# Optimization experiments

Measured on AMD Instinct MI355X. Metric: run time of the kernel, lower is better.

The kernel has to match this reference:

```python
import jax, jax.numpy as jnp
import numpy as np

B, C, H, W = 4, 64, 64, 64
C2 = 2 * C
CR = C2 // 16  # SE bottleneck

def setup_inputs() -> dict:
    key = jax.random.key(0)
    ks = jax.random.split(key, 8)
    stdv = 1.0 / np.sqrt(C)
    return {
        "x1": jax.random.normal(ks[0], (B, C, H, W), jnp.float32),
        "x2": jax.random.normal(ks[1], (B, C, H, W), jnp.float32),
        "weight": jax.random.uniform(ks[2], (C, C), jnp.float32, -stdv, stdv),
        "weight2": jax.random.uniform(ks[3], (C, C), jnp.float32, -stdv, stdv),
        "ca_fc1": jax.random.normal(ks[4], (CR, C2), jnp.float32) * 0.05,  # 1x1 conv as matrix
        "ca_fc2": jax.random.normal(ks[5], (C2, CR), jnp.float32) * 0.05,
        "conv_w": jax.random.normal(ks[6], (C, C2), jnp.float32) * 0.05,  # 1x1 conv 2C->C
        "conv_b": jnp.zeros((C,), jnp.float32),
    }

def reference(x1, x2, weight, weight2, ca_fc1, ca_fc2, conv_w, conv_b):
    b, c, h, w = x2.shape
    n = h * w
    a1 = x1.reshape(b, c, n)  # x1 flattened [B,C,N]
    a2 = x2.reshape(b, c, n)  # x2 flattened [B,C,N]
    # Non-local branch: f = theta_x @ phi_x = a1^T @ a2 -> [B,N,N]
    f = jnp.einsum('bcn,bcm->bnm', a1, a2)
    adj = jax.nn.softmax(f, axis=-1)
    support = jnp.einsum('bcn,cd->bnd', a2, weight)  # g_x @ W, [B,N,C]
    y = jnp.einsum('bnm,bmd->bnd', adj, support)     # adj @ support
    y = y.transpose(0, 2, 1).reshape(b, c, h, w)
    # Channel-affinity branch: c_x = a_x @ b_x -> [B,C,C]
    c_x = jnp.einsum('bcn,bdn->bcd', a1, a2)
    support2 = jnp.einsum('bcd,de->bce', c_x, weight2)   # [B,C,C]
    y2 = jnp.einsum('bcd,bdn->bcn', support2, a1).reshape(b, c, h, w)
    z = jnp.concatenate([y, y2], axis=1)  # [B,2C,H,W]
    # ChannelAttention: global max pool -> fc1 -> relu -> fc2 -> sigmoid
    mp = jnp.max(z, axis=(2, 3))                       # [B,2C]
    hdn = jax.nn.relu(jnp.einsum('be,re->br', mp, ca_fc1))
    v = jax.nn.sigmoid(jnp.einsum('br,er->be', hdn, ca_fc2))  # [B,2C]
    out = z * v[:, :, None, None] + z
    out = jnp.einsum('behw,oe->bohw', out, conv_w) + conv_b[None, :, None, None]
    return out
```

## Files before the change

kernel.cpp:

```cpp
#include <hip/hip_runtime.h>
#include <hip/hip_bf16.h>
#include <math.h>

#define B_   4
#define C_   64
#define N_   4096
#define C2_  128

using frag  = __attribute__((ext_vector_type(8))) short;
using f32x4 = __attribute__((ext_vector_type(4))) float;
using f4    = __attribute__((ext_vector_type(4))) float;

__device__ __forceinline__ unsigned short f2bf(float f) {
  unsigned int u = __float_as_uint(f);
  u += 0x7fffu + ((u >> 16) & 1u);
  return (unsigned short)(u >> 16);
}
__device__ __forceinline__ float bf2f(unsigned short h) {
  return __uint_as_float(((unsigned int)h) << 16);
}
__device__ __forceinline__ unsigned int pkbf(float a, float b) {
  __hip_bfloat16 ha = __float2bfloat16(a), hb = __float2bfloat16(b);
  unsigned short ua, ub;
  __builtin_memcpy(&ua, &ha, 2);
  __builtin_memcpy(&ub, &hb, 2);
  return (unsigned int)ua | ((unsigned int)ub << 16);
}
__device__ __forceinline__ frag pk8(f4 lo, f4 hi) {
  frag f;
  unsigned int* u = (unsigned int*)&f;
  u[0] = pkbf(lo.x, lo.y);
  u[1] = pkbf(lo.z, lo.w);
  u[2] = pkbf(hi.x, hi.y);
  u[3] = pkbf(hi.z, hi.w);
  return f;
}
__device__ __forceinline__ f4 max4(f4 a, f4 b) {
  return (f4){fmaxf(a.x, b.x), fmaxf(a.y, b.y), fmaxf(a.z, b.z), fmaxf(a.w, b.w)};
}

__global__ __launch_bounds__(256) void prep_kernel(const float* __restrict__ x1,
                                                   const float* __restrict__ x2,
                                                   const float* __restrict__ weight,
                                                   unsigned short* __restrict__ a1t,
                                                   unsigned short* __restrict__ a2t,
                                                   unsigned short* __restrict__ vT) {
  __shared__ float tileA[64][65];
  __shared__ float tileB[64][65];
  __shared__ float Wl[64 * 64];
  int b = blockIdx.y, n0 = blockIdx.x * 64, tid = threadIdx.x;
  int n = tid & 63;
#pragma unroll
  for (int k = 0; k < 16; ++k) {
    int lin = tid + 256 * k;
    Wl[lin] = weight[lin];
    int c = (tid >> 6) + 4 * k;
    tileA[c][n] = x2[((size_t)(b * C_ + c)) * N_ + n0 + n];
    tileB[c][n] = x1[((size_t)(b * C_ + c)) * N_ + n0 + n];
  }
  __syncthreads();
  {
    int c = tid & 63;
#pragma unroll
    for (int k = 0; k < 16; ++k) {
      int n2 = (tid >> 6) + 4 * k;
      a2t[((size_t)b * N_ + n0 + n2) * C_ + c] = f2bf(tileA[c][n2]);
      a1t[((size_t)b * N_ + n0 + n2) * C_ + c] = f2bf(tileB[c][n2]);
    }
  }
  {
    int d0 = (tid >> 6) * 16;
    float acc[16];
#pragma unroll
    for (int i = 0; i < 16; ++i) acc[i] = 0.f;
    for (int c = 0; c < 64; ++c) {
      float v = tileA[c][n];
#pragma unroll
      for (int i = 0; i < 16; ++i) acc[i] += v * Wl[c * 64 + d0 + i];
    }
#pragma unroll
    for (int i = 0; i < 16; ++i)
      vT[((size_t)(b * C_) + d0 + i) * N_ + n0 + n] = f2bf(acc[i]);
  }
}

__global__ __launch_bounds__(256) void cxmm_kernel(const float* __restrict__ x1,
                                                   const float* __restrict__ x2,
                                                   float* __restrict__ cxp) {
  int b = blockIdx.y, seg = blockIdx.x, tid = threadIdx.x;
  int wave = tid >> 6, lane = tid & 63, l16 = lane & 15, lq = lane >> 4;
  int n0 = seg * 64;
  const float* a2r = x2 + ((size_t)(b * C_) + 16 * wave + l16) * N_ + n0 + lq * 8;
  frag afr[2];
#pragma unroll
  for (int ks = 0; ks < 2; ++ks)
    afr[ks] = pk8(*(const f4*)(a2r + ks * 32), *(const f4*)(a2r + ks * 32 + 4));
  f32x4 acc[4];
#pragma unroll
  for (int cg = 0; cg < 4; ++cg) acc[cg] = (f32x4){0.f, 0.f, 0.f, 0.f};
#pragma unroll
  for (int cg = 0; cg < 4; ++cg) {
    const float* a1r = x1 + ((size_t)(b * C_) + cg * 16 + l16) * N_ + n0 + lq * 8;
#pragma unroll
    for (int ks = 0; ks < 2; ++ks) {
      frag bfr = pk8(*(const f4*)(a1r + ks * 32), *(const f4*)(a1r + ks * 32 + 4));
      acc[cg] = __builtin_amdgcn_mfma_f32_16x16x32_bf16(afr[ks], bfr, acc[cg], 0, 0, 0);
    }
  }
  float* op = cxp + ((size_t)(b * 64 + seg)) * 4096;
#pragma unroll
  for (int cg = 0; cg < 4; ++cg)
#pragma unroll
    for (int r = 0; r < 4; ++r)
      op[(16 * wave + 4 * lq + r) * 64 + cg * 16 + l16] = acc[cg][r];
}

__global__ __launch_bounds__(256) void cxred_kernel(const float* __restrict__ cxp,
                                                    float* __restrict__ cx) {
  int idx = blockIdx.x * 256 + threadIdx.x;
  int b = idx >> 12, r = idx & 4095;
  const float* p = cxp + (size_t)b * 64 * 4096 + r;
  float s = 0.f;
#pragma unroll 8
  for (int sg = 0; sg < 64; ++sg) s += p[(size_t)sg * 4096];
  cx[idx] = s;
}

__global__ __launch_bounds__(256) void s2bf_kernel(const float* __restrict__ cx,
                                                   const float* __restrict__ w2,
                                                   unsigned short* __restrict__ s2bf) {
  __shared__ float cxl[4096];
  __shared__ float w2l[4096];
  int b = blockIdx.x, tid = threadIdx.x;
#pragma unroll
  for (int k = 0; k < 16; ++k) {
    int lin = tid + 256 * k;
    cxl[lin] = cx[(size_t)b * 4096 + lin];
    w2l[lin] = w2[lin];
  }
  __syncthreads();
  int c = tid & 63, eg = tid >> 6;
  float acc[16];
#pragma unroll
  for (int i = 0; i < 16; ++i) acc[i] = 0.f;
  for (int d = 0; d < 64; ++d) {
    float a = cxl[d * 64 + c];
#pragma unroll
    for (int i = 0; i < 16; ++i) acc[i] += a * w2l[d * 64 + eg * 16 + i];
  }
  unsigned short* op = s2bf + (size_t)b * 4096 + c * 64 + eg * 16;
#pragma unroll
  for (int i = 0; i < 8; ++i)
    *(unsigned int*)(op + 2 * i) = pkbf(acc[2 * i], acc[2 * i + 1]);
}

template <int SEG>
__global__ __launch_bounds__(256) void attn_kernel(const unsigned short* __restrict__ a1t,
                                                   const unsigned short* __restrict__ a2t,
                                                   const unsigned short* __restrict__ vT,
                                                   float* __restrict__ z,
                                                   unsigned short* __restrict__ Opart,
                                                   float* __restrict__ ml) {
  __shared__ unsigned short Kt[2][64 * 64];
  __shared__ unsigned short Vt[2][64 * 64];
  __shared__ uint2 Pl[4][16 * 16];

  const int b = blockIdx.y, n0 = blockIdx.x * 64, tid = threadIdx.x;
  const int seg = (SEG > 1) ? blockIdx.z : 0;
  const int wave = tid >> 6, lane = tid & 63;
  const int l16 = lane & 15, lq = lane >> 4;
  const int NT = N_ / SEG / 64;
  const int mbase = seg * (N_ / SEG);

  const unsigned short* qbase = a1t + ((size_t)b * N_ + n0 + wave * 16 + l16) * C_;
  frag qa0 = *(const frag*)(qbase + lq * 8);
  frag qa1 = *(const frag*)(qbase + 32 + lq * 8);

  f32x4 O[4];
#pragma unroll
  for (int i = 0; i < 4; ++i) O[i] = (f32x4){0.f, 0.f, 0.f, 0.f};
  float m_l = -1e30f, l_l = 0.f;

  const unsigned short* a2b = a2t + (size_t)b * N_ * C_;
  const unsigned short* vTb = vT + (size_t)b * C_ * N_;
  char* Pw = (char*)&Pl[wave][0];
  const int swzP = (l16 & 7) << 4;

  const int srow0 = tid >> 3, scb = tid & 7;
  const int srow1 = (tid + 256) >> 3;
  const int kswz0 = (scb * 16) ^ ((srow0 & 7) << 4);
  const int kswz1 = (scb * 16) ^ ((srow1 & 7) << 4);

  frag k0 = *(const frag*)(a2b + (size_t)(mbase + srow0) * C_ + scb * 8);
  frag k1 = *(const frag*)(a2b + (size_t)(mbase + srow1) * C_ + scb * 8);
  frag v0 = *(const frag*)(vTb + (size_t)srow0 * N_ + mbase + scb * 8);
  frag v1 = *(const frag*)(vTb + (size_t)srow1 * N_ + mbase + scb * 8);
  *(frag*)((char*)&Kt[0][0] + srow0 * 128 + kswz0) = k0;
  *(frag*)((char*)&Kt[0][0] + srow1 * 128 + kswz1) = k1;
  *(frag*)((char*)&Vt[0][0] + srow0 * 128 + kswz0) = v0;
  *(frag*)((char*)&Vt[0][0] + srow1 * 128 + kswz1) = v1;
  __syncthreads();

  int cur = 0;
  for (int t = 0; t < NT; ++t, cur ^= 1) {
    if (t + 1 < NT) {
      int mn = mbase + (t + 1) * 64;
      k0 = *(const frag*)(a2b + (size_t)(mn + srow0) * C_ + scb * 8);
      k1 = *(const frag*)(a2b + (size_t)(mn + srow1) * C_ + scb * 8);
      v0 = *(const frag*)(vTb + (size_t)srow0 * N_ + mn + scb * 8);
      v1 = *(const frag*)(vTb + (size_t)srow1 * N_ + mn + scb * 8);
    }

    f32x4 S[4];
    __builtin_amdgcn_s_setprio(1);
#pragma unroll
    for (int ms = 0; ms < 4; ++ms) {
      int m = ms * 16 + l16;
      int swz = (m & 7) << 4;
      frag kb0 = *(const frag*)((char*)&Kt[cur][0] + m * 128 + ((lq * 16) ^ swz));
      frag kb1 = *(const frag*)((char*)&Kt[cur][0] + m * 128 + ((64 + lq * 16) ^ swz));
      f32x4 acc = (f32x4){0.f, 0.f, 0.f, 0.f};
      acc = __builtin_amdgcn_mfma_f32_16x16x32_bf16(kb0, qa0, acc, 0, 0, 0);
      acc = __builtin_amdgcn_mfma_f32_16x16x32_bf16(kb1, qa1, acc, 0, 0, 0);
      S[ms] = acc;
    }
    __builtin_amdgcn_s_setprio(0);

    float mx0 = fmaxf(fmaxf(S[0][0], S[0][1]), fmaxf(S[0][2], S[0][3]));
    float mx1 = fmaxf(fmaxf(S[1][0], S[1][1]), fmaxf(S[1][2], S[1][3]));
    float mx2 = fmaxf(fmaxf(S[2][0], S[2][1]), fmaxf(S[2][2], S[2][3]));
    float mx3 = fmaxf(fmaxf(S[3][0], S[3][1]), fmaxf(S[3][2], S[3][3]));
    float mx = fmaxf(fmaxf(mx0, mx1), fmaxf(mx2, mx3));
    mx = fmaxf(mx, __shfl_xor(mx, 16, 64));
    mx = fmaxf(mx, __shfl_xor(mx, 32, 64));

    if (!__all(mx <= m_l + 8.f)) {
      float mn = fmaxf(m_l, mx);
      float sc = __expf(m_l - mn);
      m_l = mn;
      l_l *= sc;
      float scb_[4];
#pragma unroll
      for (int r = 0; r < 4; ++r) scb_[r] = __shfl(sc, 20 * lq + r, 64);
#pragma unroll
      for (int ds = 0; ds < 4; ++ds)
#pragma unroll
        for (int r = 0; r < 4; ++r) O[ds][r] *= scb_[r];
    }

    float p[16];
    float rs = 0.f;
#pragma unroll
    for (int ms = 0; ms < 4; ++ms)
#pragma unroll
      for (int r = 0; r < 4; ++r) {
        float e = __expf(S[ms][r] - m_l);
        p[ms * 4 + r] = e;
        rs += e;
      }
    rs += __shfl_xor(rs, 16, 64);
    rs += __shfl_xor(rs, 32, 64);
    l_l += rs;

#pragma unroll
    for (int ms = 0; ms < 4; ++ms) {
      uint2 w;
      w.x = pkbf(p[ms * 4 + 0], p[ms * 4 + 1]);
      w.y = pkbf(p[ms * 4 + 2], p[ms * 4 + 3]);
      *(uint2*)(Pw + l16 * 128 + ((32 * ms + 8 * lq) ^ swzP)) = w;
    }
    asm volatile("s_waitcnt lgkmcnt(0)" ::: "memory");
    __builtin_amdgcn_sched_barrier(0);

    frag pa0 = *(const frag*)(Pw + l16 * 128 + ((lq * 16) ^ swzP));
    frag pa1 = *(const frag*)(Pw + l16 * 128 + ((64 + lq * 16) ^ swzP));
    __builtin_amdgcn_s_setprio(1);
#pragma unroll
    for (int ds = 0; ds < 4; ++ds) {
      int d = ds * 16 + l16;
      int swz = (d & 7) << 4;
      frag vb0 = *(const frag*)((char*)&Vt[cur][0] + d * 128 + ((lq * 16) ^ swz));
      frag vb1 = *(const frag*)((char*)&Vt[cur][0] + d * 128 + ((64 + lq * 16) ^ swz));
      O[ds] = __builtin_amdgcn_mfma_f32_16x16x32_bf16(pa0, vb0, O[ds], 0, 0, 0);
      O[ds] = __builtin_amdgcn_mfma_f32_16x16x32_bf16(pa1, vb1, O[ds], 0, 0, 0);
    }
    __builtin_amdgcn_s_setprio(0);

    if (t + 1 < NT) {
      *(frag*)((char*)&Kt[cur ^ 1][0] + srow0 * 128 + kswz0) = k0;
      *(frag*)((char*)&Kt[cur ^ 1][0] + srow1 * 128 + kswz1) = k1;
      *(frag*)((char*)&Vt[cur ^ 1][0] + srow0 * 128 + kswz0) = v0;
      *(frag*)((char*)&Vt[cur ^ 1][0] + srow1 * 128 + kswz1) = v1;
      __syncthreads();
    }
  }

  if (SEG > 1) {
    size_t base = (size_t)(b * SEG + seg) * N_ + n0 + wave * 16;
    if (lq == 0) {
      ml[(base + l16) * 2]     = m_l;
      ml[(base + l16) * 2 + 1] = l_l;
    }
#pragma unroll
    for (int r = 0; r < 4; ++r)
#pragma unroll
      for (int ds = 0; ds < 4; ++ds)
        Opart[(base + lq * 4 + r) * 64 + ds * 16 + l16] = f2bf(O[ds][r]);
  } else {
    float inv[4];
#pragma unroll
    for (int r = 0; r < 4; ++r) inv[r] = 1.f / __shfl(l_l, 20 * lq + r, 64);
#pragma unroll
    for (int ds = 0; ds < 4; ++ds)
#pragma unroll
      for (int r = 0; r < 4; ++r)
        z[((size_t)b * N_ + n0 + wave * 16 + lq * 4 + r) * 128 + ds * 16 + l16] = O[ds][r] * inv[r];
  }
}

__global__ __launch_bounds__(256) void combine_kernel(const unsigned short* __restrict__ Opart,
                                                      const float* __restrict__ ml,
                                                      float* __restrict__ z,
                                                      float* __restrict__ mppA) {
  __shared__ float zsm[64][65];
  int b = blockIdx.y, tid = threadIdx.x;
  int nr = tid >> 2;
  int n = blockIdx.x * 64 + nr;
  int dq = (tid & 3) * 16;
  float mv[4], lv[4], M = -1e30f;
#pragma unroll
  for (int s = 0; s < 4; ++s) {
    size_t r = (size_t)(b * 4 + s) * N_ + n;
    mv[s] = ml[r * 2];
    lv[s] = ml[r * 2 + 1];
    M = fmaxf(M, mv[s]);
  }
  float acc[16];
#pragma unroll
  for (int j = 0; j < 16; ++j) acc[j] = 0.f;
  float l = 0.f;
#pragma unroll
  for (int s = 0; s < 4; ++s) {
    float w = __expf(mv[s] - M);
    l += w * lv[s];
    const unsigned short* op = Opart + ((size_t)(b * 4 + s) * N_ + n) * 64 + dq;
    frag p0 = *(const frag*)(op);
    frag p1 = *(const frag*)(op + 8);
#pragma unroll
    for (int j = 0; j < 8; ++j) {
      acc[j]     += w * bf2f((unsigned short)p0[j]);
      acc[8 + j] += w * bf2f((unsigned short)p1[j]);
    }
  }
  float inv = 1.f / l;
  float* zp = z + ((size_t)b * N_ + n) * 128 + dq;
#pragma unroll
  for (int k = 0; k < 4; ++k) {
    f4 res = (f4){acc[4 * k] * inv, acc[4 * k + 1] * inv,
                  acc[4 * k + 2] * inv, acc[4 * k + 3] * inv};
    *(f4*)(zp + k * 4) = res;
    zsm[nr][dq + 4 * k]     = res.x;
    zsm[nr][dq + 4 * k + 1] = res.y;
    zsm[nr][dq + 4 * k + 2] = res.z;
    zsm[nr][dq + 4 * k + 3] = res.w;
  }
  __syncthreads();
  if (tid < 64) {
    float mx = -1e30f;
    for (int nn = 0; nn < 64; ++nn) mx = fmaxf(mx, zsm[nn][tid]);
    mppA[((size_t)b * 64 + blockIdx.x) * 64 + tid] = mx;
  }
}

__global__ __launch_bounds__(256) void mpA_kernel(const float* __restrict__ z,
                                                  float* __restrict__ mppA) {
  __shared__ float red[4][64];
  int b = blockIdx.y, n0 = blockIdx.x * 64, tid = threadIdx.x;
  int e = tid & 63, g = tid >> 6;
  float mx = -1e30f;
#pragma unroll
  for (int k = 0; k < 16; ++k)
    mx = fmaxf(mx, z[((size_t)b * N_ + n0 + g + 4 * k) * 128 + e]);
  red[g][e] = mx;
  __syncthreads();
  if (tid < 64)
    mppA[((size_t)b * 64 + blockIdx.x) * 64 + tid] =
        fmaxf(fmaxf(red[0][tid], red[1][tid]), fmaxf(red[2][tid], red[3][tid]));
}

__global__ __launch_bounds__(256) void y2_kernel(const unsigned short* __restrict__ s2bf,
                                                 const unsigned short* __restrict__ a1t,
                                                 float* __restrict__ z,
                                                 float* __restrict__ mppB) {
  __shared__ f4 red[4][4][16];
  int b = blockIdx.y, n0 = blockIdx.x * 32, tid = threadIdx.x;
  int wave = tid >> 6, lane = tid & 63, l16 = lane & 15, lq = lane >> 4;
  const unsigned short* s2r = s2bf + (size_t)b * 4096 + (16 * wave + l16) * 64;
  frag sa0 = *(const frag*)(s2r + lq * 8);
  frag sa1 = *(const frag*)(s2r + 32 + lq * 8);
  f4 mx = (f4){-1e30f, -1e30f, -1e30f, -1e30f};
#pragma unroll
  for (int j = 0; j < 2; ++j) {
    const unsigned short* bp = a1t + ((size_t)b * N_ + n0 + 16 * j + l16) * 64;
    frag b0 = *(const frag*)(bp + lq * 8);
    frag b1 = *(const frag*)(bp + 32 + lq * 8);
    f32x4 acc = (f32x4){0.f, 0.f, 0.f, 0.f};
    acc = __builtin_amdgcn_mfma_f32_16x16x32_bf16(sa0, b0, acc, 0, 0, 0);
    acc = __builtin_amdgcn_mfma_f32_16x16x32_bf16(sa1, b1, acc, 0, 0, 0);
    *(f4*)(z + ((size_t)b * N_ + n0 + 16 * j + l16) * 128 + 64 + 16 * wave + 4 * lq) = acc;
#pragma unroll
    for (int r = 0; r < 4; ++r) mx[r] = fmaxf(mx[r], acc[r]);
  }
  red[wave][lq][l16] = mx;
  __syncthreads();
  if (tid < 64) {
    int w = tid >> 4, q = (tid >> 2) & 3, r = tid & 3;
    float m = -1e30f;
#pragma unroll
    for (int l = 0; l < 16; ++l) m = fmaxf(m, red[w][q][l][r]);
    mppB[((size_t)b * 128 + blockIdx.x) * 64 + 16 * w + 4 * q + r] = m;
  }
}

__global__ __launch_bounds__(256) void ca2_kernel(const float* __restrict__ mppA,
                                                  const float* __restrict__ mppB,
                                                  const float* __restrict__ fc1,
                                                  const float* __restrict__ fc2,
                                                  float* __restrict__ vbuf) {
  __shared__ f4 red4[256];
  __shared__ float mpl[128];
  __shared__ float red2[8][33];
  __shared__ float hl[8];
  int b = blockIdx.x, t = threadIdx.x;
  {
    const f4* src = (const f4*)(mppA + (size_t)b * 64 * 64);
    f4 m = src[t];
    m = max4(m, src[t + 256]);
    m = max4(m, src[t + 512]);
    m = max4(m, src[t + 768]);
    red4[t] = m;
  }
  __syncthreads();
  if (t < 16) {
    f4 m = red4[t];
#pragma unroll
    for (int j = 1; j < 16; ++j) m = max4(m, red4[t + 16 * j]);
    *(f4*)&mpl[t * 4] = m;
  }
  __syncthreads();
  {
    const f4* src = (const f4*)(mppB + (size_t)b * 128 * 64);
    f4 m = src[t];
#pragma unroll
    for (int k = 1; k < 8; ++k) m = max4(m, src[t + 256 * k]);
    red4[t] = m;
  }
  __syncthreads();
  if (t < 16) {
    f4 m = red4[t];
#pragma unroll
    for (int j = 1; j < 16; ++j) m = max4(m, red4[t + 16 * j]);
    *(f4*)&mpl[64 + t * 4] = m;
  }
  __syncthreads();
  {
    int r = t >> 5, j = t & 31;
    const f4 mv = *(const f4*)&mpl[j * 4];
    const f4 wv = *(const f4*)(fc1 + r * 128 + j * 4);
    red2[r][j] = mv.x * wv.x + mv.y * wv.y + mv.z * wv.z + mv.w * wv.w;
  }
  __syncthreads();
  if (t < 8) {
    float s = 0.f;
#pragma unroll
    for (int j = 0; j < 32; ++j) s += red2[t][j];
    hl[t] = fmaxf(s, 0.f);
  }
  __syncthreads();
  if (t < 128) {
    float s = 0.f;
    const float* f2r = fc2 + t * 8;
#pragma unroll
    for (int r = 0; r < 8; ++r) s += hl[r] * f2r[r];
    vbuf[b * 128 + t] = 1.f + 1.f / (1.f + __expf(-s));
  }
}

__global__ __launch_bounds__(256) void conv_kernel(const float* __restrict__ z,
                                                   const float* __restrict__ vbuf,
                                                   const float* __restrict__ conv_w,
                                                   const float* __restrict__ conv_b,
                                                   float* __restrict__ out) {
  __shared__ unsigned short zv[64 * 128];
  int b = blockIdx.y, n0 = blockIdx.x * 64, tid = threadIdx.x;
  int wave = tid >> 6, lane = tid & 63, l16 = lane & 15, lq = lane >> 4;
  {
    int e4 = tid & 31;
    f4 vq = *(const f4*)(vbuf + b * 128 + e4 * 4);
#pragma unroll
    for (int k = 0; k < 8; ++k) {
      int row = (tid >> 5) + 8 * k;
      f4 zq = *(const f4*)(z + ((size_t)(b * N_) + n0 + row) * 128 + e4 * 4);
      zq *= vq;
      uint2 w;
      w.x = pkbf(zq.x, zq.y);
      w.y = pkbf(zq.z, zq.w);
      *(uint2*)((char*)zv + row * 256 + ((e4 * 8) ^ ((row & 7) << 4))) = w;
    }
  }
  const float* cwr = conv_w + (size_t)(16 * wave + l16) * 128 + lq * 8;
  frag aw[4];
#pragma unroll
  for (int ks = 0; ks < 4; ++ks)
    aw[ks] = pk8(*(const f4*)(cwr + ks * 32), *(const f4*)(cwr + ks * 32 + 4));
  __syncthreads();
  f32x4 acc[4];
#pragma unroll
  for (int ng = 0; ng < 4; ++ng) acc[ng] = (f32x4){0.f, 0.f, 0.f, 0.f};
#pragma unroll
  for (int ng = 0; ng < 4; ++ng) {
    int n = ng * 16 + l16;
    int swz = (n & 7) << 4;
#pragma unroll
    for (int ks = 0; ks < 4; ++ks) {
      frag bz = *(const frag*)((char*)zv + n * 256 + ((ks * 64 + lq * 16) ^ swz));
      acc[ng] = __builtin_amdgcn_mfma_f32_16x16x32_bf16(aw[ks], bz, acc[ng], 0, 0, 0);
    }
  }
#pragma unroll
  for (int r = 0; r < 4; ++r) {
    int o = 16 * wave + 4 * lq + r;
    float bias = conv_b[o];
#pragma unroll
    for (int ng = 0; ng < 4; ++ng)
      out[((size_t)(b * C_ + o)) * N_ + n0 + ng * 16 + l16] = acc[ng][r] + bias;
  }
}

extern "C" void kernel_launch(void* const* d_in, const int* in_sizes, int n_in,
                              void* d_out, int out_size, void* d_ws, size_t ws_size,
                              hipStream_t stream) {
  const float* x1      = (const float*)d_in[0];
  const float* x2      = (const float*)d_in[1];
  const float* weight  = (const float*)d_in[2];
  const float* weight2 = (const float*)d_in[3];
  const float* fc1     = (const float*)d_in[4];
  const float* fc2     = (const float*)d_in[5];
  const float* conv_w  = (const float*)d_in[6];
  const float* conv_b  = (const float*)d_in[7];
  float* out = (float*)d_out;

  char* ws = (char*)d_ws;
  unsigned short* a1t = (unsigned short*)(ws + 0);
  unsigned short* a2t = (unsigned short*)(ws + 2097152);
  float* mppA = (float*)(ws + 2097152);
  float* mppB = (float*)(ws + 2162688);
  unsigned short* s2bf = (unsigned short*)(ws + 2293760);
  unsigned short* vT  = (unsigned short*)(ws + 4194304);
  float* z    = (float*)(ws + 6291456);
  float* cxp  = (float*)(ws + 6291456);
  float* cx   = (float*)(ws + 14680064);
  float* vbuf = (float*)(ws + 14745600);
  unsigned short* Opart = (unsigned short*)(ws + 14764544);
  float* ml   = (float*)(ws + 23153152);
  const bool seg4 = ws_size >= 23677440ull;

  cxmm_kernel<<<dim3(64, 4), 256, 0, stream>>>(x1, x2, cxp);
  prep_kernel<<<dim3(64, 4), 256, 0, stream>>>(x1, x2, weight, a1t, a2t, vT);
  cxred_kernel<<<dim3(64), 256, 0, stream>>>(cxp, cx);
  if (seg4) {
    attn_kernel<4><<<dim3(64, 4, 4), 256, 0, stream>>>(a1t, a2t, vT, z, Opart, ml);
    combine_kernel<<<dim3(64, 4), 256, 0, stream>>>(Opart, ml, z, mppA);
  } else {
    attn_kernel<1><<<dim3(64, 4), 256, 0, stream>>>(a1t, a2t, vT, z, nullptr, nullptr);
    mpA_kernel<<<dim3(64, 4), 256, 0, stream>>>(z, mppA);
  }
  s2bf_kernel<<<dim3(4), 256, 0, stream>>>(cx, weight2, s2bf);
  y2_kernel<<<dim3(128, 4), 256, 0, stream>>>(s2bf, a1t, z, mppB);
  ca2_kernel<<<dim3(4), 256, 0, stream>>>(mppA, mppB, fc1, fc2, vbuf);
  conv_kernel<<<dim3(64, 4), 256, 0, stream>>>(z, vbuf, conv_w, conv_b, out);
}
```

Before: 83.29 us.

## Split prep into transpose kernel and MFMA-based support matmul kernel

The fused prep kernel previously transposed x1/x2 to bf16 and computed x2^T·W with scalar FMAs from shared memory. It is now split into a lighter transpose kernel with half-size tiles (more blocks) and a separate kernel that computes the support product with bf16 MFMA instructions reading the transposed a2t. This aims to remove the scalar FMA loop and raise parallelism, at the cost of an extra launch, a re-read of a2t, and bf16 rounding of W and x2 before the product.

```diff
diff --git a/kernel.cpp b/kernel.cpp
--- a/kernel.cpp
+++ b/kernel.cpp
@@ -41,47 +41,73 @@
 
 __global__ __launch_bounds__(256) void prep_kernel(const float* __restrict__ x1,
                                                    const float* __restrict__ x2,
-                                                   const float* __restrict__ weight,
                                                    unsigned short* __restrict__ a1t,
-                                                   unsigned short* __restrict__ a2t,
-                                                   unsigned short* __restrict__ vT) {
-  __shared__ float tileA[64][65];
-  __shared__ float tileB[64][65];
-  __shared__ float Wl[64 * 64];
-  int b = blockIdx.y, n0 = blockIdx.x * 64, tid = threadIdx.x;
-  int n = tid & 63;
+                                                   unsigned short* __restrict__ a2t) {
+  __shared__ float tA[64 * 33];
+  __shared__ float tB[64 * 33];
+  int b = blockIdx.y, n0 = blockIdx.x * 32, tid = threadIdx.x;
+  {
+    int n = tid & 31, cq = tid >> 5;
+#pragma unroll
+    for (int k = 0; k < 8; ++k) {
+      int c = cq + 8 * k;
+      tA[c * 33 + n] = x2[((size_t)(b * C_ + c)) * N_ + n0 + n];
+      tB[c * 33 + n] = x1[((size_t)(b * C_ + c)) * N_ + n0 + n];
+    }
+  }
+  __syncthreads();
+  {
+    int c = tid & 63, nq = tid >> 6;
+#pragma unroll
+    for (int k = 0; k < 8; ++k) {
+      int n2 = nq + 4 * k;
+      a2t[((size_t)b * N_ + n0 + n2) * C_ + c] = f2bf(tA[c * 33 + n2]);
+      a1t[((size_t)b * N_ + n0 + n2) * C_ + c] = f2bf(tB[c * 33 + n2]);
+    }
+  }
+}
+
+__global__ __launch_bounds__(256) void support_mm_kernel(const float* __restrict__ weight,
+                                                         const unsigned short* __restrict__ a2t,
+                                                         unsigned short* __restrict__ vT) {
+  __shared__ float Wl[64 * 65];
+  int b = blockIdx.y, n0 = blockIdx.x * 32, tid = threadIdx.x;
+  int wave = tid >> 6, lane = tid & 63, l16 = lane & 15, lq = lane >> 4;
 #pragma unroll
   for (int k = 0; k < 16; ++k) {
     int lin = tid + 256 * k;
-    Wl[lin] = weight[lin];
-    int c = (tid >> 6) + 4 * k;
-    tileA[c][n] = x2[((size_t)(b * C_ + c)) * N_ + n0 + n];
-    tileB[c][n] = x1[((size_t)(b * C_ + c)) * N_ + n0 + n];
-  }
-  __syncthreads();
-  {
-    int c = tid & 63;
-#pragma unroll
-    for (int k = 0; k < 16; ++k) {
-      int n2 = (tid >> 6) + 4 * k;
-      a2t[((size_t)b * N_ + n0 + n2) * C_ + c] = f2bf(tileA[c][n2]);
-      a1t[((size_t)b * N_ + n0 + n2) * C_ + c] = f2bf(tileB[c][n2]);
-    }
-  }
-  {
-    int d0 = (tid >> 6) * 16;
-    float acc[16];
-#pragma unroll
-    for (int i = 0; i < 16; ++i) acc[i] = 0.f;
-    for (int c = 0; c < 64; ++c) {
-      float v = tileA[c][n];
-#pragma unroll
-      for (int i = 0; i < 16; ++i) acc[i] += v * Wl[c * 64 + d0 + i];
-    }
-#pragma unroll
-    for (int i = 0; i < 16; ++i)
-      vT[((size_t)(b * C_) + d0 + i) * N_ + n0 + n] = f2bf(acc[i]);
-  }
+    Wl[(lin >> 6) * 65 + (lin & 63)] = weight[lin];
+  }
+  frag b0[2], b1[2];
+#pragma unroll
+  for (int ng = 0; ng < 2; ++ng) {
+    const unsigned short* bp = a2t + ((size_t)b * N_ + n0 + ng * 16 + l16) * C_;
+    b0[ng] = *(const frag*)(bp + lq * 8);
+    b1[ng] = *(const frag*)(bp + 32 + lq * 8);
+  }
+  __syncthreads();
+  int dd = 16 * wave + l16;
+  frag aw[2];
+#pragma unroll
+  for (int ks = 0; ks < 2; ++ks) {
+    float wv[8];
+#pragma unroll
+    for (int j = 0; j < 8; ++j) wv[j] = Wl[(ks * 32 + lq * 8 + j) * 65 + dd];
+    aw[ks] = pk8((f4){wv[0], wv[1], wv[2], wv[3]}, (f4){wv[4], wv[5], wv[6], wv[7]});
+  }
+  f32x4 acc[2];
+#pragma unroll
+  for (int ng = 0; ng < 2; ++ng) {
+    acc[ng] = (f32x4){0.f, 0.f, 0.f, 0.f};
+    acc[ng] = __builtin_amdgcn_mfma_f32_16x16x32_bf16(aw[0], b0[ng], acc[ng], 0, 0, 0);
+    acc[ng] = __builtin_amdgcn_mfma_f32_16x16x32_bf16(aw[1], b1[ng], acc[ng], 0, 0, 0);
+  }
+#pragma unroll
+  for (int ng = 0; ng < 2; ++ng)
+#pragma unroll
+    for (int r = 0; r < 4; ++r)
+      vT[((size_t)(b * C_) + 16 * wave + 4 * lq + r) * N_ + n0 + ng * 16 + l16] =
+          f2bf(acc[ng][r]);
 }
 
 __global__ __launch_bounds__(256) void cxmm_kernel(const float* __restrict__ x1,
@@ -566,7 +592,8 @@
   const bool seg4 = ws_size >= 23677440ull;
 
   cxmm_kernel<<<dim3(64, 4), 256, 0, stream>>>(x1, x2, cxp);
-  prep_kernel<<<dim3(64, 4), 256, 0, stream>>>(x1, x2, weight, a1t, a2t, vT);
+  prep_kernel<<<dim3(128, 4), 256, 0, stream>>>(x1, x2, a1t, a2t);
+  support_mm_kernel<<<dim3(128, 4), 256, 0, stream>>>(weight, a2t, vT);
   cxred_kernel<<<dim3(64), 256, 0, stream>>>(cxp, cx);
   if (seg4) {
     attn_kernel<4><<<dim3(64, 4, 4), 256, 0, stream>>>(a1t, a2t, vT, z, Opart, ml);
```

After: 81.83 us. Within noise of the previous version (-1.7%).
